# Optimization experiments

Hardware: AMD Instinct MI355X
Metric: run time of the kernel (lower is better)

Reference implementation:

```python
import jax, jax.numpy as jnp
import numpy as np

# Typical Deformable-DETR pyramid for an 800x1200 image, strides 8/16/32/64
SPATIAL = np.array([[100, 150], [50, 75], [25, 38], [13, 19]], dtype=np.int64)


def setup_inputs() -> dict:
    key = jax.random.key(0)
    k1, k2, k3 = jax.random.split(key, 3)
    bs, heads, d, L, P = 2, 8, 32, 4, 4
    num_keys = int((SPATIAL[:, 0] * SPATIAL[:, 1]).sum())  # 18947
    Q = num_keys  # encoder self-attention: one query per key
    value = jax.random.normal(k1, (bs, num_keys, heads, d), dtype=jnp.float32)
    # normalized sampling coords in [0,1] (module maps to [-1,1] via 2*x-1)
    sampling_locations = jax.random.uniform(k2, (bs, Q, heads, L, P, 2), dtype=jnp.float32)
    w = jax.random.uniform(k3, (bs, Q, heads, L, P), dtype=jnp.float32)
    attention_weights = jax.nn.softmax(w.reshape(bs, Q, heads, L * P), axis=-1).reshape(bs, Q, heads, L, P)
    return {
        "value": value,
        "value_spatial_shapes": jnp.asarray(SPATIAL),
        "sampling_locations": sampling_locations,
        "attention_weights": attention_weights,
    }


def _bilinear_sample(v, grid):
    """F.grid_sample(mode='bilinear', padding_mode='zeros', align_corners=False).
    v: (N, H, W, d); grid: (N, Q, P, 2) with (x, y) in [-1, 1].
    Returns (N, Q, P, d)."""
    N, H, W, d = v.shape
    x = (grid[..., 0] + 1.0) * (W * 0.5) - 0.5
    y = (grid[..., 1] + 1.0) * (H * 0.5) - 0.5
    x0 = jnp.floor(x).astype(jnp.int32)
    y0 = jnp.floor(y).astype(jnp.int32)
    x1, y1 = x0 + 1, y0 + 1
    wx1 = x - x0
    wy1 = y - y0
    wx0 = 1.0 - wx1
    wy0 = 1.0 - wy1
    nidx = jnp.arange(N)[:, None, None]

    def gather(yy, xx):
        m = ((xx >= 0) & (xx < W) & (yy >= 0) & (yy < H)).astype(v.dtype)
        out = v[nidx, jnp.clip(yy, 0, H - 1), jnp.clip(xx, 0, W - 1)]  # (N,Q,P,d)
        return out * m[..., None]

    return (gather(y0, x0) * (wy0 * wx0)[..., None]
            + gather(y0, x1) * (wy0 * wx1)[..., None]
            + gather(y1, x0) * (wy1 * wx0)[..., None]
            + gather(y1, x1) * (wy1 * wx1)[..., None])


def reference(value, value_spatial_shapes, sampling_locations, attention_weights):
    shapes = np.asarray(value_spatial_shapes)  # static level shapes
    bs, num_keys, heads, d = value.shape
    _, Q, _, L, P, _ = sampling_locations.shape
    grids = 2.0 * sampling_locations - 1.0  # (bs,Q,heads,L,P,2)
    sampled = []
    start = 0
    for lvl in range(L):
        H, W = int(shapes[lvl, 0]), int(shapes[lvl, 1])
        v = value[:, start:start + H * W]  # (bs, H*W, heads, d)
        start += H * W
        v = v.transpose(0, 2, 1, 3).reshape(bs * heads, H, W, d)
        g = grids[:, :, :, lvl].transpose(0, 2, 1, 3, 4).reshape(bs * heads, Q, P, 2)
        sampled.append(_bilinear_sample(v, g))  # (bs*heads, Q, P, d)
    s = jnp.stack(sampled, axis=2)  # (bs*heads, Q, L, P, d)
    w = attention_weights.transpose(0, 2, 1, 3, 4).reshape(bs * heads, Q, L, P)
    out = jnp.einsum('nqlpd,nqlp->nqd', s, w)  # (bs*heads, Q, d)
    # feature layout matches torch: channel index = head*d + c
    return out.reshape(bs, heads, Q, d).transpose(0, 2, 1, 3).reshape(bs, Q, heads * d)
```

## Files before the change

### kernel.cpp

```cpp
#include <hip/hip_runtime.h>
#include <hip/hip_fp16.h>


#define KQ 19947
#define NBQ (2 * KQ)

__global__ __launch_bounds__(256) void transpose_f16(
    const float* __restrict__ V, __half* __restrict__ Vh)
{
    const int pair = blockIdx.y;
    const int j = blockIdx.x * 256 + threadIdx.x;
    if (j >= KQ * 4) return;
    const int k = j >> 2, cg = j & 3;
    const int b = pair >> 3, h = pair & 7;
    const float* src = V + (((size_t)b * KQ + k) * 8 + h) * 32 + cg * 8;
    const float4 a0 = *reinterpret_cast<const float4*>(src);
    const float4 a1 = *reinterpret_cast<const float4*>(src + 4);
    __half2 h0 = __floats2half2_rn(a0.x, a0.y);
    __half2 h1 = __floats2half2_rn(a0.z, a0.w);
    __half2 h2 = __floats2half2_rn(a1.x, a1.y);
    __half2 h3 = __floats2half2_rn(a1.z, a1.w);
    uint4 o;
    o.x = *reinterpret_cast<unsigned int*>(&h0);
    o.y = *reinterpret_cast<unsigned int*>(&h1);
    o.z = *reinterpret_cast<unsigned int*>(&h2);
    o.w = *reinterpret_cast<unsigned int*>(&h3);
    reinterpret_cast<uint4*>(Vh + ((size_t)pair * KQ) * 32)[j] = o;
}

template<int L>
static __device__ __forceinline__ void addr_level(
    const float* __restrict__ lp, const float* __restrict__ wp,
    float slotf, int* off, float* cw)
{
    constexpr int Hh = (L == 0) ? 100 : (L == 1) ? 50 : (L == 2) ? 25 : 13;
    constexpr int Ww = (L == 0) ? 150 : (L == 1) ? 75 : (L == 2) ? 38 : 19;
    constexpr int st = (L == 0) ? 0 : (L == 1) ? 15000 : (L == 2) ? 18750 : 19700;
    const float Hf = (float)Hh, Wf = (float)Ww;
    const float4 w4 = *reinterpret_cast<const float4*>(wp + L * 4);
    const float4 g0 = *reinterpret_cast<const float4*>(lp + L * 8);
    const float4 g1 = *reinterpret_cast<const float4*>(lp + L * 8 + 4);
    const float lx[4] = {g0.x, g0.z, g1.x, g1.z};
    const float ly[4] = {g0.y, g0.w, g1.y, g1.w};
    const float ww[4] = {w4.x, w4.y, w4.z, w4.w};
    #pragma unroll
    for (int p = 0; p < 4; ++p) {
        const float x = fmaf(lx[p], Wf, -0.5f);
        const float y = fmaf(ly[p], Hf, -0.5f);
        const float fy = floorf(y);
        const int y0 = (int)fy;
        const int x0 = (int)floorf(x);
        const int bx = min(max(x0, 0), Ww - 2);
        const float wxl = fmaxf(0.f, 1.f - fabsf(x - ((float)bx + slotf)));
        const float wy1 = y - fy, wy0 = 1.f - wy1;
        const int y0c = max(y0, 0);
        const int y1c = min(y0 + 1, Hh - 1);
        const float ay0 = (y0 >= 0)     ? wy0 : 0.f;
        const float ay1 = (y0 + 1 < Hh) ? wy1 : 0.f;
        const float wl = ww[p] * wxl;
        off[2*p]   = (st + y0c * Ww + bx) << 5;
        off[2*p+1] = (st + y1c * Ww + bx) << 5;
        cw[2*p]    = wl * ay0;
        cw[2*p+1]  = wl * ay1;
    }
}

static __device__ __forceinline__ void consume_level(
    const uint4* v, const float* cw, float acc[8])
{
    __half2 accH[4];
    #pragma unroll
    for (int j = 0; j < 4; ++j) accH[j] = __half2(__half(0.f), __half(0.f));
    #pragma unroll
    for (int i = 0; i < 8; ++i) {
        const __half2 wh = __floats2half2_rn(cw[i], cw[i]);
        union { uint4 u; __half2 h2[4]; } uv;
        uv.u = v[i];
        #pragma unroll
        for (int j = 0; j < 4; ++j)
            accH[j] = __hfma2(wh, uv.h2[j], accH[j]);
    }
    #pragma unroll
    for (int j = 0; j < 4; ++j) {
        const float2 f = __half22float2(accH[j]);
        acc[2*j]   += f.x;
        acc[2*j+1] += f.y;
    }
}

#define GLOAD8(buf, obase)                                                   \
    {                                                                        \
        _Pragma("unroll")                                                    \
        for (int i = 0; i < 8; ++i) {                                        \
            const __half* p_ = vbl + (obase)[i];                             \
            asm volatile("global_load_dwordx4 %0, %1, off"                   \
                         : "=v"(buf[i]) : "v"(p_));                          \
        }                                                                    \
    }
#define VWAIT(n)                                                             \
    asm volatile("s_waitcnt vmcnt(" #n ")" ::: "memory");                    \
    __builtin_amdgcn_sched_barrier(0)
#define SBAR() __builtin_amdgcn_sched_barrier(0)

__global__ __launch_bounds__(256, 3) void msda_fwd_t(
    const __half* __restrict__ Vh,
    const float* __restrict__ LOC,
    const float* __restrict__ W,
    float* __restrict__ OUT)
{
    const int pair = blockIdx.x & 15;
    const int qc   = blockIdx.x >> 4;
    const int tid  = threadIdx.x;
    const int s    = tid & 7;
    const int slot = s >> 2;
    const float slotf = (float)slot;
    const int q    = qc * 32 + (tid >> 3);
    if (q >= KQ) return;
    const int b = pair >> 3, h = pair & 7;

    const __half* vbl = Vh + (size_t)pair * KQ * 32 + s * 8;
    const float* lp = LOC + (((size_t)b * KQ + q) * 8 + h) * 32;
    const float* wp = W   + (((size_t)b * KQ + q) * 8 + h) * 16;

    float acc[8];
    #pragma unroll
    for (int c = 0; c < 8; ++c) acc[c] = 0.f;

    int off[32];
    float cw[32];
    addr_level<0>(lp, wp, slotf, off + 0,  cw + 0);
    addr_level<1>(lp, wp, slotf, off + 8,  cw + 8);
    addr_level<2>(lp, wp, slotf, off + 16, cw + 16);
    addr_level<3>(lp, wp, slotf, off + 24, cw + 24);

    VWAIT(0);

    uint4 va[8], vb2[8], vc[8];
    GLOAD8(va,  off + 0);
    GLOAD8(vb2, off + 8);
    VWAIT(8);
    GLOAD8(vc,  off + 16);
    SBAR();
    consume_level(va, cw + 0, acc);
    SBAR();
    GLOAD8(va,  off + 24);
    VWAIT(16);
    consume_level(vb2, cw + 8, acc);
    VWAIT(8);
    consume_level(vc, cw + 16, acc);
    VWAIT(0);
    consume_level(va, cw + 24, acc);

    #pragma unroll
    for (int c = 0; c < 8; ++c)
        acc[c] += __shfl_xor(acc[c], 4, 64);

    float* op = OUT + ((size_t)b * KQ + q) * 256 + h * 32 + (s & 3) * 8 + slot * 4;
    *reinterpret_cast<float4*>(op) =
        make_float4(acc[slot*4], acc[slot*4+1], acc[slot*4+2], acc[slot*4+3]);
}

static __device__ __forceinline__ void fmadd4(float4& a, float s, const float4 v) {
    a.x = fmaf(s, v.x, a.x);
    a.y = fmaf(s, v.y, a.y);
    a.z = fmaf(s, v.z, a.z);
    a.w = fmaf(s, v.w, a.w);
}

__global__ __launch_bounds__(256, 4) void msda_fwd_f32(
    const float* __restrict__ V,
    const float* __restrict__ LOC,
    const float* __restrict__ W,
    float* __restrict__ OUT)
{
    const int t  = blockIdx.x * 256 + threadIdx.x;
    const int cg = t & 7;
    const int h  = (t >> 3) & 7;
    const int bq = t >> 6;
    if (bq >= NBQ) return;
    const int b = (bq >= KQ) ? 1 : 0;

    const int Hs[4]  = {100, 50, 25, 13};
    const int Ws[4]  = {150, 75, 38, 19};
    const int STs[4] = {0, 15000, 18750, 19700};

    const int hoff = (h << 5) + (cg << 2);
    const float* vb = V + (size_t)b * KQ * 256 + hoff;
    const float* lp = LOC + ((size_t)bq * 8 + h) * 32;
    const float* wp = W   + ((size_t)bq * 8 + h) * 16;

    float4 acc = make_float4(0.f, 0.f, 0.f, 0.f);

    #pragma unroll
    for (int l = 0; l < 4; ++l) {
        const int Hh = Hs[l], Ww = Ws[l], st = STs[l];
        const float Hf = (float)Hh, Wf = (float)Ww;
        const float4 w4 = *reinterpret_cast<const float4*>(wp + l * 4);
        const float4 g0 = *reinterpret_cast<const float4*>(lp + l * 8);
        const float4 g1 = *reinterpret_cast<const float4*>(lp + l * 8 + 4);
        const float lx[4] = {g0.x, g0.z, g1.x, g1.z};
        const float ly[4] = {g0.y, g0.w, g1.y, g1.w};
        const float ww[4] = {w4.x, w4.y, w4.z, w4.w};
        #pragma unroll
        for (int p = 0; p < 4; ++p) {
            const float x = fmaf(lx[p], Wf, -0.5f);
            const float y = fmaf(ly[p], Hf, -0.5f);
            const float fx = floorf(x), fy = floorf(y);
            const int x0 = (int)fx, y0 = (int)fy;
            const float wx1 = x - fx, wy1 = y - fy;
            const float wx0 = 1.f - wx1, wy0 = 1.f - wy1;
            const int x0c = max(x0, 0),     x1c = min(x0 + 1, Ww - 1);
            const int y0c = max(y0, 0),     y1c = min(y0 + 1, Hh - 1);
            const float ax0 = (x0 >= 0)      ? wx0 : 0.f;
            const float ax1 = (x0 + 1 < Ww)  ? wx1 : 0.f;
            const float ay0 = (y0 >= 0)      ? wy0 : 0.f;
            const float ay1 = (y0 + 1 < Hh)  ? wy1 : 0.f;
            const float w = ww[p];
            const int b0 = st + y0c * Ww, b1 = st + y1c * Ww;
            fmadd4(acc, w*ay0*ax0, *reinterpret_cast<const float4*>(vb + ((b0+x0c) << 8)));
            fmadd4(acc, w*ay0*ax1, *reinterpret_cast<const float4*>(vb + ((b0+x1c) << 8)));
            fmadd4(acc, w*ay1*ax0, *reinterpret_cast<const float4*>(vb + ((b1+x0c) << 8)));
            fmadd4(acc, w*ay1*ax1, *reinterpret_cast<const float4*>(vb + ((b1+x1c) << 8)));
        }
    }
    *reinterpret_cast<float4*>(OUT + (size_t)bq * 256 + hoff) = acc;
}

extern "C" void kernel_launch(void* const* d_in, const int* in_sizes, int n_in,
                              void* d_out, int out_size, void* d_ws, size_t ws_size,
                              hipStream_t stream) {
    const float* V   = (const float*)d_in[0];
    const float* LOC = (const float*)d_in[2];
    const float* W   = (const float*)d_in[3];
    float* OUT = (float*)d_out;

    const size_t n_val = (size_t)2 * KQ * 256;
    const size_t need  = n_val * sizeof(__half) + 256;

    if (ws_size >= need) {
        __half* Vh = (__half*)d_ws;
        const int jtot = KQ * 4;
        dim3 tgrid((jtot + 255) / 256, 16);
        hipLaunchKernelGGL(transpose_f16, tgrid, dim3(256), 0, stream, V, Vh);

        const int qchunks = (KQ + 31) / 32;
        const int blocks  = qchunks * 16;
        hipLaunchKernelGGL(msda_fwd_t, dim3(blocks), dim3(256), 0, stream,
                           Vh, LOC, W, OUT);
    } else {
        const int total = NBQ * 64;
        hipLaunchKernelGGL(msda_fwd_f32, dim3((total + 255) / 256), dim3(256), 0, stream,
                           V, LOC, W, OUT);
    }
}
```

Baseline: 88.45 us.

## Process two queries per thread with double-buffered per-level pipelined gathers

Each thread now handles two queries, and the grid is halved to match. Sampling locations and weights are loaded one level at a time with inline asm, and the corner gathers are double-buffered so one level's loads overlap the previous level's accumulation. Addressing switches to an SGPR base plus a 32-bit VGPR byte offset, and only 8 offsets are live at once instead of 32, which lowers register pressure. In exchange each thread runs a longer serial chain of loads and the grid has fewer blocks, so less latency can be hidden across waves.

```diff
diff --git a/kernel.cpp b/kernel.cpp
--- a/kernel.cpp
+++ b/kernel.cpp
@@ -30,19 +30,16 @@
 
 template<int L>
 static __device__ __forceinline__ void addr_level(
-    const float* __restrict__ lp, const float* __restrict__ wp,
-    float slotf, int* off, float* cw)
+    float4 pg0, float4 pg1, float4 pw,
+    float slotf, int g_base, int* off, float* cw)
 {
     constexpr int Hh = (L == 0) ? 100 : (L == 1) ? 50 : (L == 2) ? 25 : 13;
     constexpr int Ww = (L == 0) ? 150 : (L == 1) ? 75 : (L == 2) ? 38 : 19;
     constexpr int st = (L == 0) ? 0 : (L == 1) ? 15000 : (L == 2) ? 18750 : 19700;
     const float Hf = (float)Hh, Wf = (float)Ww;
-    const float4 w4 = *reinterpret_cast<const float4*>(wp + L * 4);
-    const float4 g0 = *reinterpret_cast<const float4*>(lp + L * 8);
-    const float4 g1 = *reinterpret_cast<const float4*>(lp + L * 8 + 4);
-    const float lx[4] = {g0.x, g0.z, g1.x, g1.z};
-    const float ly[4] = {g0.y, g0.w, g1.y, g1.w};
-    const float ww[4] = {w4.x, w4.y, w4.z, w4.w};
+    const float lx[4] = {pg0.x, pg0.z, pg1.x, pg1.z};
+    const float ly[4] = {pg0.y, pg0.w, pg1.y, pg1.w};
+    const float ww[4] = {pw.x, pw.y, pw.z, pw.w};
     #pragma unroll
     for (int p = 0; p < 4; ++p) {
         const float x = fmaf(lx[p], Wf, -0.5f);
@@ -58,15 +55,15 @@
         const float ay0 = (y0 >= 0)     ? wy0 : 0.f;
         const float ay1 = (y0 + 1 < Hh) ? wy1 : 0.f;
         const float wl = ww[p] * wxl;
-        off[2*p]   = (st + y0c * Ww + bx) << 5;
-        off[2*p+1] = (st + y1c * Ww + bx) << 5;
+        off[2*p]   = ((st + y0c * Ww + bx) << 6) + g_base;
+        off[2*p+1] = ((st + y1c * Ww + bx) << 6) + g_base;
         cw[2*p]    = wl * ay0;
         cw[2*p+1]  = wl * ay1;
     }
 }
 
 static __device__ __forceinline__ void consume_level(
-    const uint4* v, const float* cw, float acc[8])
+    const uint4* v, const float* cw, float* acc)
 {
     __half2 accH[4];
     #pragma unroll
@@ -88,19 +85,25 @@
     }
 }
 
-#define GLOAD8(buf, obase)                                                   \
+#define PLOAD(l, lbase, wbase)                                               \
+    asm volatile("global_load_dwordx4 %0, %1, %2"                            \
+                 : "=v"(pg0) : "v"((lbase) + (l) * 32), "s"(LOC));           \
+    asm volatile("global_load_dwordx4 %0, %1, %2"                            \
+                 : "=v"(pg1) : "v"((lbase) + (l) * 32 + 16), "s"(LOC));      \
+    asm volatile("global_load_dwordx4 %0, %1, %2"                            \
+                 : "=v"(pw)  : "v"((wbase) + (l) * 16), "s"(W))
+
+#define GLOAD8(buf)                                                          \
     {                                                                        \
         _Pragma("unroll")                                                    \
-        for (int i = 0; i < 8; ++i) {                                        \
-            const __half* p_ = vbl + (obase)[i];                             \
-            asm volatile("global_load_dwordx4 %0, %1, off"                   \
-                         : "=v"(buf[i]) : "v"(p_));                          \
-        }                                                                    \
-    }
+        for (int i = 0; i < 8; ++i)                                          \
+            asm volatile("global_load_dwordx4 %0, %1, %2"                    \
+                         : "=v"(buf[i]) : "v"(off[i]), "s"(Vh));             \
+    }
+
 #define VWAIT(n)                                                             \
     asm volatile("s_waitcnt vmcnt(" #n ")" ::: "memory");                    \
     __builtin_amdgcn_sched_barrier(0)
-#define SBAR() __builtin_amdgcn_sched_barrier(0)
 
 __global__ __launch_bounds__(256, 3) void msda_fwd_t(
     const __half* __restrict__ Vh,
@@ -114,50 +117,97 @@
     const int s    = tid & 7;
     const int slot = s >> 2;
     const float slotf = (float)slot;
-    const int q    = qc * 32 + (tid >> 3);
-    if (q >= KQ) return;
+    const int q0   = qc * 64 + (tid >> 3);
+    const int q1   = q0 + 32;
+    const int q1c  = min(q1, KQ - 1);
     const int b = pair >> 3, h = pair & 7;
 
-    const __half* vbl = Vh + (size_t)pair * KQ * 32 + s * 8;
-    const float* lp = LOC + (((size_t)b * KQ + q) * 8 + h) * 32;
-    const float* wp = W   + (((size_t)b * KQ + q) * 8 + h) * 16;
-
-    float acc[8];
-    #pragma unroll
-    for (int c = 0; c < 8; ++c) acc[c] = 0.f;
-
-    int off[32];
-    float cw[32];
-    addr_level<0>(lp, wp, slotf, off + 0,  cw + 0);
-    addr_level<1>(lp, wp, slotf, off + 8,  cw + 8);
-    addr_level<2>(lp, wp, slotf, off + 16, cw + 16);
-    addr_level<3>(lp, wp, slotf, off + 24, cw + 24);
-
+    const int g_base = pair * KQ * 64 + s * 16;
+    const int lb0 = (((b * KQ + q0) * 8) + h) << 7;
+    const int wb0 = (((b * KQ + q0) * 8) + h) << 6;
+    const int lb1 = (((b * KQ + q1c) * 8) + h) << 7;
+    const int wb1 = (((b * KQ + q1c) * 8) + h) << 6;
+
+    float acc0[8], acc1[8];
+    #pragma unroll
+    for (int c = 0; c < 8; ++c) { acc0[c] = 0.f; acc1[c] = 0.f; }
+
+    float4 pg0, pg1, pw;
+    int off[8];
+    uint4 bufA[8], bufB[8];
+    float cwA[8], cwB[8];
+
+    PLOAD(0, lb0, wb0);
     VWAIT(0);
-
-    uint4 va[8], vb2[8], vc[8];
-    GLOAD8(va,  off + 0);
-    GLOAD8(vb2, off + 8);
-    VWAIT(8);
-    GLOAD8(vc,  off + 16);
-    SBAR();
-    consume_level(va, cw + 0, acc);
-    SBAR();
-    GLOAD8(va,  off + 24);
-    VWAIT(16);
-    consume_level(vb2, cw + 8, acc);
-    VWAIT(8);
-    consume_level(vc, cw + 16, acc);
+    addr_level<0>(pg0, pg1, pw, slotf, g_base, off, cwA);
+    PLOAD(1, lb0, wb0);
+    GLOAD8(bufA);
+    VWAIT(8);
+
+    addr_level<1>(pg0, pg1, pw, slotf, g_base, off, cwB);
+    PLOAD(2, lb0, wb0);
+    GLOAD8(bufB);
+    VWAIT(11);
+    consume_level(bufA, cwA, acc0);
+    VWAIT(8);
+
+    addr_level<2>(pg0, pg1, pw, slotf, g_base, off, cwA);
+    PLOAD(3, lb0, wb0);
+    GLOAD8(bufA);
+    VWAIT(11);
+    consume_level(bufB, cwB, acc0);
+    VWAIT(8);
+
+    addr_level<3>(pg0, pg1, pw, slotf, g_base, off, cwB);
+    PLOAD(0, lb1, wb1);
+    GLOAD8(bufB);
+    VWAIT(11);
+    consume_level(bufA, cwA, acc0);
+    VWAIT(8);
+
+    addr_level<0>(pg0, pg1, pw, slotf, g_base, off, cwA);
+    PLOAD(1, lb1, wb1);
+    GLOAD8(bufA);
+    VWAIT(11);
+    consume_level(bufB, cwB, acc0);
+    VWAIT(8);
+
+    addr_level<1>(pg0, pg1, pw, slotf, g_base, off, cwB);
+    PLOAD(2, lb1, wb1);
+    GLOAD8(bufB);
+    VWAIT(11);
+    consume_level(bufA, cwA, acc1);
+    VWAIT(8);
+
+    addr_level<2>(pg0, pg1, pw, slotf, g_base, off, cwA);
+    PLOAD(3, lb1, wb1);
+    GLOAD8(bufA);
+    VWAIT(11);
+    consume_level(bufB, cwB, acc1);
+    VWAIT(8);
+
+    addr_level<3>(pg0, pg1, pw, slotf, g_base, off, cwB);
+    GLOAD8(bufB);
+    VWAIT(8);
+    consume_level(bufA, cwA, acc1);
     VWAIT(0);
-    consume_level(va, cw + 24, acc);
-
-    #pragma unroll
-    for (int c = 0; c < 8; ++c)
-        acc[c] += __shfl_xor(acc[c], 4, 64);
-
-    float* op = OUT + ((size_t)b * KQ + q) * 256 + h * 32 + (s & 3) * 8 + slot * 4;
-    *reinterpret_cast<float4*>(op) =
-        make_float4(acc[slot*4], acc[slot*4+1], acc[slot*4+2], acc[slot*4+3]);
+    consume_level(bufB, cwB, acc1);
+
+    #pragma unroll
+    for (int c = 0; c < 8; ++c) {
+        acc0[c] += __shfl_xor(acc0[c], 4, 64);
+        acc1[c] += __shfl_xor(acc1[c], 4, 64);
+    }
+
+    const int co = h * 32 + (s & 3) * 8 + slot * 4;
+    float* op0 = OUT + ((size_t)b * KQ + q0) * 256 + co;
+    *reinterpret_cast<float4*>(op0) =
+        make_float4(acc0[slot*4], acc0[slot*4+1], acc0[slot*4+2], acc0[slot*4+3]);
+    if (q1 < KQ) {
+        float* op1 = OUT + ((size_t)b * KQ + q1) * 256 + co;
+        *reinterpret_cast<float4*>(op1) =
+            make_float4(acc1[slot*4], acc1[slot*4+1], acc1[slot*4+2], acc1[slot*4+3]);
+    }
 }
 
 static __device__ __forceinline__ void fmadd4(float4& a, float s, const float4 v) {
@@ -243,7 +293,7 @@
         dim3 tgrid((jtot + 255) / 256, 16);
         hipLaunchKernelGGL(transpose_f16, tgrid, dim3(256), 0, stream, V, Vh);
 
-        const int qchunks = (KQ + 31) / 32;
+        const int qchunks = (KQ + 63) / 64;
         const int blocks  = qchunks * 16;
         hipLaunchKernelGGL(msda_fwd_t, dim3(blocks), dim3(256), 0, stream,
                            Vh, LOC, W, OUT);
```

New measurement: 90.15 us. Within noise of the previous version (+1.9%).
